# Performance work log

Hardware: AMD Instinct MI355X
Metric: run time of the kernel (lower is better)

## Reference

```python
import jax, jax.numpy as jnp
import numpy as np

N_BOX = 1000000


def box2corners(box):
    # box: (N,5) = x,y,w,h,alpha -> corners (N,4,2), order matches lilanxiao/Rotated_IoU
    x, y, w, h, a = (box[:, i] for i in range(5))
    dx = jnp.array([0.5, -0.5, -0.5, 0.5], box.dtype)
    dy = jnp.array([0.5, 0.5, -0.5, -0.5], box.dtype)
    cx = dx[None, :] * w[:, None]
    cy = dy[None, :] * h[:, None]
    c, s = jnp.cos(a)[:, None], jnp.sin(a)[:, None]
    rx = cx * c - cy * s + x[:, None]
    ry = cx * s + cy * c + y[:, None]
    return jnp.stack([rx, ry], axis=-1)


def edge_intersections(c1, c2):
    # all 4x4 edge-pair intersections; strict interior criterion (0<t<1, 0<u<1)
    p1, p2 = c1, jnp.roll(c1, -1, axis=1)
    p3, p4 = c2, jnp.roll(c2, -1, axis=1)
    x1, y1 = p1[:, :, None, 0], p1[:, :, None, 1]
    x2, y2 = p2[:, :, None, 0], p2[:, :, None, 1]
    x3, y3 = p3[:, None, :, 0], p3[:, None, :, 1]
    x4, y4 = p4[:, None, :, 0], p4[:, None, :, 1]
    num_t = (x2 - x1) * (y3 - y1) - (y2 - y1) * (x3 - x1)
    den_t = (x2 - x1) * (y3 - y4) - (y2 - y1) * (x3 - x4)
    t = jnp.where(den_t == 0., -1., num_t / jnp.where(den_t == 0., 1., den_t))
    mask_t = (t > 0.) & (t < 1.)
    num_u = (x4 - x3) * (y1 - y3) - (y4 - y3) * (x1 - x3)
    den_u = (x4 - x3) * (y1 - y2) - (y4 - y3) * (x1 - x2)
    u = jnp.where(den_u == 0., -1., num_u / jnp.where(den_u == 0., 1., den_u))
    mask = mask_t & (u > 0.) & (u < 1.)
    tx = x1 + t * (x2 - x1)
    ty = y1 + t * (y2 - y1)
    pts = jnp.stack([tx, ty], axis=-1) * mask[..., None]
    n = c1.shape[0]
    return pts.reshape(n, 16, 2), mask.reshape(n, 16)


def box_in_box(corners1, corners2):
    # projection test: is each corner of box1 inside rectangle box2
    a = corners2[:, 0:1, :]
    b = corners2[:, 1:2, :]
    d = corners2[:, 3:4, :]
    ab, ad, am = b - a, d - a, corners1 - a
    p_ab = (ab * am).sum(-1) / (ab * ab).sum(-1)
    p_ad = (ad * am).sum(-1) / (ad * ad).sum(-1)
    eps = 1e-6
    return (p_ab > -eps) & (p_ab < 1. + eps) & (p_ad > -eps) & (p_ad < 1. + eps)


def intersection_area(c1, c2):
    # convex intersection polygon: 24 candidate vertices, sort valid ones by angle, shoelace
    pts, m_int = edge_intersections(c1, c2)
    m1 = box_in_box(c1, c2)
    m2 = box_in_box(c2, c1)
    verts = jnp.concatenate([c1, c2, pts], axis=1)   # (N,24,2)
    mask = jnp.concatenate([m1, m2, m_int], axis=1)  # (N,24)
    k = mask.sum(axis=1)
    mean = (verts * mask[..., None]).sum(1, keepdims=True) / jnp.maximum(k, 1)[:, None, None]
    v = jnp.where(mask[..., None], verts - mean, 0.)
    ang = jnp.where(mask, jnp.arctan2(v[..., 1], v[..., 0]), 1e9)
    order = jnp.argsort(ang, axis=1)
    vs = jnp.take_along_axis(v, order[..., None], axis=1)
    pad = jnp.arange(24)[None, :, None] < k[:, None, None]
    vs = jnp.where(pad, vs, vs[:, 0:1, :])  # pad by repeating first valid vertex -> zero cross terms
    vn = jnp.roll(vs, -1, axis=1)
    cross = vs[..., 0] * vn[..., 1] - vs[..., 1] * vn[..., 0]
    return 0.5 * jnp.abs(cross.sum(axis=1))


def riou_loss(pred, target):
    # RIOUloss(reduction='none', loss_type='iou') -> cal_diou per-box loss, loss[0]
    rad_p = jnp.arctan2(pred[:, 4], pred[:, 5])
    rad_t = jnp.arctan2(target[:, 4], target[:, 5])
    b1 = jnp.concatenate([pred[:, :4], rad_p[:, None]], axis=1)
    b2 = jnp.concatenate([target[:, :4], rad_t[:, None]], axis=1)
    c1 = box2corners(b1)
    c2 = box2corners(b2)
    inter = intersection_area(c1, c2)
    area1 = b1[:, 2] * b1[:, 3]
    area2 = b2[:, 2] * b2[:, 3]
    union = area1 + area2 - inter
    iou = inter / union
    allc = jnp.concatenate([c1, c2], axis=1)  # (N,8,2) enclosing box (axis-aligned)
    wc = allc[..., 0].max(1) - allc[..., 0].min(1)
    hc = allc[..., 1].max(1) - allc[..., 1].min(1)
    c2diag = wc * wc + hc * hc
    d2 = (b1[:, 0] - b2[:, 0]) ** 2 + (b1[:, 1] - b2[:, 1]) ** 2
    return 1. - iou + d2 / c2diag


def setup_inputs() -> dict:
    key = jax.random.key(0)
    k1, k2, k3, k4 = jax.random.split(key, 4)
    n = N_BOX
    xy = jax.random.uniform(k1, (n, 2)) * 640.
    wh = jax.random.uniform(k2, (n, 2)) * 48. + 2.
    sc = jax.random.normal(k3, (n, 2)) + 0.1
    pred = jnp.concatenate([xy, wh, sc], axis=1)
    k5, k6, k7 = jax.random.split(k4, 3)
    t_xy = xy + jax.random.normal(k5, (n, 2)) * 8.
    t_wh = jnp.abs(wh * (1. + 0.2 * jax.random.normal(k6, (n, 2)))) + 1.
    t_sc = sc + 0.3 * jax.random.normal(k7, (n, 2))
    target = jnp.concatenate([t_xy, t_wh, t_sc], axis=1)
    return {"pred": pred, "target": target}


def reference(pred, target):
    return riou_loss(pred, target)
```

## Files before the change

### kernel.cpp

```cpp
#include <hip/hip_runtime.h>
#include <math.h>


#define FMUL __fmul_rn
#define FADD __fadd_rn
#define FSUB __fsub_rn
#define FDIV __fdiv_rn

__device__ __forceinline__ float rcpf_(float x) { return __builtin_amdgcn_rcpf(x); }

__global__
__attribute__((amdgpu_flat_work_group_size(256, 256), amdgpu_waves_per_eu(1)))
void riou_kernel(const float* __restrict__ pred,
                 const float* __restrict__ tgt,
                 float* __restrict__ out, int n)
{
    int i = blockIdx.x * blockDim.x + threadIdx.x;
    if (i >= n) return;

    const float2* p2 = (const float2*)(pred + 6 * (size_t)i);
    const float2* q2 = (const float2*)(tgt  + 6 * (size_t)i);
    float2 pa = p2[0], pb = p2[1], pc2 = p2[2];
    float2 qa = q2[0], qb = q2[1], qc2 = q2[2];
    const float px = pa.x, py = pa.y, pw = pb.x, ph = pb.y;
    const float qx = qa.x, qy = qa.y, qw = qb.x, qh = qb.y;

    float rad1 = atan2f(pc2.x, pc2.y);
    float cA = cosf(rad1), sA = sinf(rad1);
    float rad2 = atan2f(qc2.x, qc2.y);
    float cB = cosf(rad2), sB = sinf(rad2);

    const float ddx[4] = {0.5f, -0.5f, -0.5f, 0.5f};
    const float ddy[4] = {0.5f, 0.5f, -0.5f, -0.5f};
    float c1x[4], c1y[4], c2x[4], c2y[4];
#pragma unroll
    for (int j = 0; j < 4; j++) {
        float cx = FMUL(ddx[j], pw), cy = FMUL(ddy[j], ph);
        c1x[j] = FADD(FSUB(FMUL(cx, cA), FMUL(cy, sA)), px);
        c1y[j] = FADD(FADD(FMUL(cx, sA), FMUL(cy, cA)), py);
        float dx2 = FMUL(ddx[j], qw), dy2 = FMUL(ddy[j], qh);
        c2x[j] = FADD(FSUB(FMUL(dx2, cB), FMUL(dy2, sB)), qx);
        c2y[j] = FADD(FADD(FMUL(dx2, sB), FMUL(dy2, cB)), qy);
    }

    float minx = c1x[0], maxx = c1x[0], miny = c1y[0], maxy = c1y[0];
#pragma unroll
    for (int j = 1; j < 4; j++) {
        minx = fminf(minx, c1x[j]); maxx = fmaxf(maxx, c1x[j]);
        miny = fminf(miny, c1y[j]); maxy = fmaxf(maxy, c1y[j]);
    }
#pragma unroll
    for (int j = 0; j < 4; j++) {
        minx = fminf(minx, c2x[j]); maxx = fmaxf(maxx, c2x[j]);
        miny = fminf(miny, c2y[j]); maxy = fmaxf(maxy, c2y[j]);
    }
    float wcb = FSUB(maxx, minx), hcb = FSUB(maxy, miny);
    float c2d = FADD(FMUL(wcb, wcb), FMUL(hcb, hcb));
    float dxc = FSUB(px, qx), dyc = FSUB(py, qy);
    float d2 = FADD(FMUL(dxc, dxc), FMUL(dyc, dyc));

    float vx[24], vy[24];
    unsigned mbits = 0;
    float sx = 0.0f, sy = 0.0f;
    const float eps = 1e-6f;
    const float hieps = 1.0f + 1e-6f;

    {
        float ax = c2x[0], ay = c2y[0];
        float abx = FSUB(c2x[1], ax), aby = FSUB(c2y[1], ay);
        float adx = FSUB(c2x[3], ax), ady = FSUB(c2y[3], ay);
        float rab = rcpf_(FADD(FMUL(abx, abx), FMUL(aby, aby)));
        float rad = rcpf_(FADD(FMUL(adx, adx), FMUL(ady, ady)));
#pragma unroll
        for (int j = 0; j < 4; j++) {
            float amx = FSUB(c1x[j], ax), amy = FSUB(c1y[j], ay);
            float pab = FMUL(FADD(FMUL(abx, amx), FMUL(aby, amy)), rab);
            float pad = FMUL(FADD(FMUL(adx, amx), FMUL(ady, amy)), rad);
            int m = (pab > -eps) & (pab < hieps) & (pad > -eps) & (pad < hieps);
            vx[j] = c1x[j]; vy[j] = c1y[j];
            mbits |= (unsigned)m << j;
            sx = FADD(sx, m ? c1x[j] : 0.0f);
            sy = FADD(sy, m ? c1y[j] : 0.0f);
        }
    }
    {
        float ax = c1x[0], ay = c1y[0];
        float abx = FSUB(c1x[1], ax), aby = FSUB(c1y[1], ay);
        float adx = FSUB(c1x[3], ax), ady = FSUB(c1y[3], ay);
        float rab = rcpf_(FADD(FMUL(abx, abx), FMUL(aby, aby)));
        float rad = rcpf_(FADD(FMUL(adx, adx), FMUL(ady, ady)));
#pragma unroll
        for (int j = 0; j < 4; j++) {
            float amx = FSUB(c2x[j], ax), amy = FSUB(c2y[j], ay);
            float pab = FMUL(FADD(FMUL(abx, amx), FMUL(aby, amy)), rab);
            float pad = FMUL(FADD(FMUL(adx, amx), FMUL(ady, amy)), rad);
            int m = (pab > -eps) & (pab < hieps) & (pad > -eps) & (pad < hieps);
            vx[4 + j] = c2x[j]; vy[4 + j] = c2y[j];
            mbits |= (unsigned)m << (4 + j);
            sx = FADD(sx, m ? c2x[j] : 0.0f);
            sy = FADD(sy, m ? c2y[j] : 0.0f);
        }
    }
    float fex[4], fey[4];
#pragma unroll
    for (int e2 = 0; e2 < 4; e2++) {
        fex[e2] = FSUB(c2x[(e2 + 1) & 3], c2x[e2]);
        fey[e2] = FSUB(c2y[(e2 + 1) & 3], c2y[e2]);
    }
#pragma unroll
    for (int e1 = 0; e1 < 4; e1++) {
        float x1 = c1x[e1], y1 = c1y[e1];
        float ex = FSUB(c1x[(e1 + 1) & 3], x1), ey = FSUB(c1y[(e1 + 1) & 3], y1);
#pragma unroll
        for (int e2 = 0; e2 < 4; e2++) {
            float dx31 = FSUB(c2x[e2], x1), dy31 = FSUB(c2y[e2], y1);
            float num_t = FSUB(FMUL(ex, dy31), FMUL(ey, dx31));
            float den_t = FSUB(FMUL(ey, fex[e2]), FMUL(ex, fey[e2]));
            float rd = rcpf_(den_t);
            float tq = FMUL(num_t, rd);
            float num_u = FSUB(FMUL(fey[e2], dx31), FMUL(fex[e2], dy31));
            float uq = FMUL(num_u, rd);
            int m = (tq > 0.0f) & (tq < 1.0f) & (uq < 0.0f) & (uq > -1.0f);
            float ix = FADD(x1, FMUL(tq, ex));
            float iy = FADD(y1, FMUL(tq, ey));
            int s = 8 + 4 * e1 + e2;
            vx[s] = ix; vy[s] = iy;
            mbits |= (unsigned)m << s;
            sx = FADD(sx, m ? ix : 0.0f);
            sy = FADD(sy, m ? iy : 0.0f);
        }
    }

    int k = __popc(mbits);

    float kk = (float)(k > 0 ? k : 1);
    float mx = FDIV(sx, kk), my = FDIV(sy, kk);

    unsigned pk[24];
#pragma unroll
    for (int j = 0; j < 24; j++) {
        int m = (mbits >> j) & 1u;
        float wx2 = FSUB(vx[j], mx);
        float wy2 = FSUB(vy[j], my);
        vx[j] = wx2; vy[j] = wy2;
        float dsum = FADD(fabsf(wx2), fabsf(wy2));
        float rs = (dsum > 0.0f) ? FMUL(wx2, rcpf_(dsum)) : 1.0f;
        float keyf = copysignf(FSUB(1.0f, rs), wy2);
        unsigned sb = __float_as_uint(keyf);
        unsigned u = sb ^ (unsigned)(((int)sb >> 31) | (int)0x80000000);
        pk[j] = m ? ((u & 0xFFFFFFE0u) | (unsigned)j)
                  : (0xFFFFFFE0u | (unsigned)j);
    }

    unsigned prevkey = 0xFFFFFFFFu;
    float firstx = 0.0f, firsty = 0.0f, prevx = 0.0f, prevy = 0.0f;
    float crs = 0.0f;
#pragma unroll
    for (int s = 0; s < 8; s++) {
        unsigned poff = prevkey + 1u;
        unsigned cb0, cb1, cb2, cb3;
        float cxx0, cxx1, cxx2, cxx3, cyy0, cyy1, cyy2, cyy3;
#pragma unroll
        for (int c = 0; c < 4; c++) {
            unsigned b = pk[6 * c] - poff;
            float bx = vx[6 * c], by = vy[6 * c];
#pragma unroll
            for (int t = 1; t < 6; t++) {
                int j = 6 * c + t;
                unsigned wj = pk[j] - poff;
                bool lt = wj < b;
                b  = lt ? wj : b;
                bx = lt ? vx[j] : bx;
                by = lt ? vy[j] : by;
            }
            if (c == 0) { cb0 = b; cxx0 = bx; cyy0 = by; }
            else if (c == 1) { cb1 = b; cxx1 = bx; cyy1 = by; }
            else if (c == 2) { cb2 = b; cxx2 = bx; cyy2 = by; }
            else { cb3 = b; cxx3 = bx; cyy3 = by; }
        }
        bool l01 = cb1 < cb0;
        unsigned b01 = l01 ? cb1 : cb0;
        float x01 = l01 ? cxx1 : cxx0, y01 = l01 ? cyy1 : cyy0;
        bool l23 = cb3 < cb2;
        unsigned b23 = l23 ? cb3 : cb2;
        float x23 = l23 ? cxx3 : cxx2, y23 = l23 ? cyy3 : cyy2;
        bool lf = b23 < b01;
        unsigned bw = lf ? b23 : b01;
        float bx = lf ? x23 : x01, by = lf ? y23 : y01;
        unsigned bestkey = bw + poff;
        bool act = s < k;
        bx = act ? bx : prevx;
        by = act ? by : prevy;
        if (s == 0) { firstx = bx; firsty = by; }
        else {
            crs = FADD(crs, FSUB(FMUL(prevx, by), FMUL(prevy, bx)));
        }
        prevx = bx; prevy = by; prevkey = bestkey;
    }
    for (int s = 8; s < k; s++) {
        unsigned poff = prevkey + 1u;
        unsigned best = pk[0] - poff;
        float bx = vx[0], by = vy[0];
#pragma unroll
        for (int j = 1; j < 24; j++) {
            unsigned wj = pk[j] - poff;
            bool lt = wj < best;
            best = lt ? wj : best;
            bx = lt ? vx[j] : bx;
            by = lt ? vy[j] : by;
        }
        crs = FADD(crs, FSUB(FMUL(prevx, by), FMUL(prevy, bx)));
        prevx = bx; prevy = by; prevkey = best + poff;
    }
    crs = FADD(crs, FSUB(FMUL(prevx, firsty), FMUL(prevy, firstx)));
    float inter = FMUL(0.5f, fabsf(crs));

    float area1 = FMUL(pw, ph), area2 = FMUL(qw, qh);
    float uni = FSUB(FADD(area1, area2), inter);
    float iou = FMUL(inter, rcpf_(uni));

    out[i] = FADD(FSUB(1.0f, iou), FMUL(d2, rcpf_(c2d)));
}

extern "C" void kernel_launch(void* const* d_in, const int* in_sizes, int n_in,
                              void* d_out, int out_size, void* d_ws, size_t ws_size,
                              hipStream_t stream) {
    const float* pred = (const float*)d_in[0];
    const float* tgt  = (const float*)d_in[1];
    float* out = (float*)d_out;
    int n = in_sizes[0] / 6;
    int block = 256;
    int grid = (n + block - 1) / block;
    riou_kernel<<<grid, block, 0, stream>>>(pred, tgt, out, n);
}
```

Before: 127.9 us.

## Replace repeated selection with sorting network and stage vertices in LDS

Replaces the 8-round full min-selection over 24 packed angle keys with a sorting network: three sorted groups of 8, merged to keep the lowest 8, then vertices are gathered by index. Vertex coordinates move from register arrays into a per-thread shared-memory array so they can be fetched by the sorted index without carrying x/y through every compare. The goal is fewer compare-select instructions and less register pressure. The cost is extra LDS stores and loads. The rare case of more than 8 vertices falls back to a min-search over the remaining keys, which removes each chosen key after use.

```diff
diff --git a/kernel.cpp b/kernel.cpp
--- a/kernel.cpp
+++ b/kernel.cpp
@@ -8,6 +8,23 @@
 #define FDIV __fdiv_rn
 
 __device__ __forceinline__ float rcpf_(float x) { return __builtin_amdgcn_rcpf(x); }
+
+#define CE(A,B) do { unsigned _x = pk[A], _y = pk[B]; \
+                     pk[A] = _x < _y ? _x : _y; pk[B] = _x < _y ? _y : _x; } while (0)
+
+#define SORT8(o) do { \
+    CE(o+0,o+1); CE(o+2,o+3); CE(o+0,o+2); CE(o+1,o+3); CE(o+1,o+2); \
+    CE(o+4,o+5); CE(o+6,o+7); CE(o+4,o+6); CE(o+5,o+7); CE(o+5,o+6); \
+    CE(o+0,o+4); CE(o+1,o+5); CE(o+2,o+6); CE(o+3,o+7); \
+    CE(o+2,o+4); CE(o+3,o+5); \
+    CE(o+1,o+2); CE(o+3,o+4); CE(o+5,o+6); } while (0)
+
+#define MERGE_LOW8(o) do { \
+    CE(0,o+7); CE(1,o+6); CE(2,o+5); CE(3,o+4); \
+    CE(4,o+3); CE(5,o+2); CE(6,o+1); CE(7,o+0); \
+    CE(0,4); CE(1,5); CE(2,6); CE(3,7); \
+    CE(0,2); CE(1,3); CE(4,6); CE(5,7); \
+    CE(0,1); CE(2,3); CE(4,5); CE(6,7); } while (0)
 
 __global__
 __attribute__((amdgpu_flat_work_group_size(256, 256), amdgpu_waves_per_eu(1)))
@@ -15,7 +32,9 @@
                  const float* __restrict__ tgt,
                  float* __restrict__ out, int n)
 {
-    int i = blockIdx.x * blockDim.x + threadIdx.x;
+    __shared__ float2 vlds[24][256];
+    const int tid = threadIdx.x;
+    int i = blockIdx.x * blockDim.x + tid;
     if (i >= n) return;
 
     const float2* p2 = (const float2*)(pred + 6 * (size_t)i);
@@ -59,7 +78,6 @@
     float dxc = FSUB(px, qx), dyc = FSUB(py, qy);
     float d2 = FADD(FMUL(dxc, dxc), FMUL(dyc, dyc));
 
-    float vx[24], vy[24];
     unsigned mbits = 0;
     float sx = 0.0f, sy = 0.0f;
     const float eps = 1e-6f;
@@ -77,7 +95,6 @@
             float pab = FMUL(FADD(FMUL(abx, amx), FMUL(aby, amy)), rab);
             float pad = FMUL(FADD(FMUL(adx, amx), FMUL(ady, amy)), rad);
             int m = (pab > -eps) & (pab < hieps) & (pad > -eps) & (pad < hieps);
-            vx[j] = c1x[j]; vy[j] = c1y[j];
             mbits |= (unsigned)m << j;
             sx = FADD(sx, m ? c1x[j] : 0.0f);
             sy = FADD(sy, m ? c1y[j] : 0.0f);
@@ -95,7 +112,6 @@
             float pab = FMUL(FADD(FMUL(abx, amx), FMUL(aby, amy)), rab);
             float pad = FMUL(FADD(FMUL(adx, amx), FMUL(ady, amy)), rad);
             int m = (pab > -eps) & (pab < hieps) & (pad > -eps) & (pad < hieps);
-            vx[4 + j] = c2x[j]; vy[4 + j] = c2y[j];
             mbits |= (unsigned)m << (4 + j);
             sx = FADD(sx, m ? c2x[j] : 0.0f);
             sy = FADD(sy, m ? c2y[j] : 0.0f);
@@ -124,7 +140,7 @@
             float ix = FADD(x1, FMUL(tq, ex));
             float iy = FADD(y1, FMUL(tq, ey));
             int s = 8 + 4 * e1 + e2;
-            vx[s] = ix; vy[s] = iy;
+            vlds[s][tid] = make_float2(ix, iy);
             mbits |= (unsigned)m << s;
             sx = FADD(sx, m ? ix : 0.0f);
             sy = FADD(sy, m ? iy : 0.0f);
@@ -140,9 +156,13 @@
 #pragma unroll
     for (int j = 0; j < 24; j++) {
         int m = (mbits >> j) & 1u;
-        float wx2 = FSUB(vx[j], mx);
-        float wy2 = FSUB(vy[j], my);
-        vx[j] = wx2; vy[j] = wy2;
+        float rx, ry;
+        if (j < 4)      { rx = c1x[j];     ry = c1y[j];     }
+        else if (j < 8) { rx = c2x[j - 4]; ry = c2y[j - 4]; }
+        else            { float2 v = vlds[j][tid]; rx = v.x; ry = v.y; }
+        float wx2 = FSUB(rx, mx);
+        float wy2 = FSUB(ry, my);
+        vlds[j][tid] = make_float2(wx2, wy2);
         float dsum = FADD(fabsf(wx2), fabsf(wy2));
         float rs = (dsum > 0.0f) ? FMUL(wx2, rcpf_(dsum)) : 1.0f;
         float keyf = copysignf(FSUB(1.0f, rs), wy2);
@@ -152,65 +172,43 @@
                   : (0xFFFFFFE0u | (unsigned)j);
     }
 
-    unsigned prevkey = 0xFFFFFFFFu;
+    SORT8(0);
+    SORT8(8);
+    SORT8(16);
+    MERGE_LOW8(8);
+    MERGE_LOW8(16);
+
+    float gxv[8], gyv[8];
+#pragma unroll
+    for (int s = 0; s < 8; s++) {
+        float2 v = vlds[pk[s] & 31u][tid];
+        gxv[s] = v.x; gyv[s] = v.y;
+    }
+
     float firstx = 0.0f, firsty = 0.0f, prevx = 0.0f, prevy = 0.0f;
     float crs = 0.0f;
 #pragma unroll
     for (int s = 0; s < 8; s++) {
-        unsigned poff = prevkey + 1u;
-        unsigned cb0, cb1, cb2, cb3;
-        float cxx0, cxx1, cxx2, cxx3, cyy0, cyy1, cyy2, cyy3;
-#pragma unroll
-        for (int c = 0; c < 4; c++) {
-            unsigned b = pk[6 * c] - poff;
-            float bx = vx[6 * c], by = vy[6 * c];
-#pragma unroll
-            for (int t = 1; t < 6; t++) {
-                int j = 6 * c + t;
-                unsigned wj = pk[j] - poff;
-                bool lt = wj < b;
-                b  = lt ? wj : b;
-                bx = lt ? vx[j] : bx;
-                by = lt ? vy[j] : by;
-            }
-            if (c == 0) { cb0 = b; cxx0 = bx; cyy0 = by; }
-            else if (c == 1) { cb1 = b; cxx1 = bx; cyy1 = by; }
-            else if (c == 2) { cb2 = b; cxx2 = bx; cyy2 = by; }
-            else { cb3 = b; cxx3 = bx; cyy3 = by; }
-        }
-        bool l01 = cb1 < cb0;
-        unsigned b01 = l01 ? cb1 : cb0;
-        float x01 = l01 ? cxx1 : cxx0, y01 = l01 ? cyy1 : cyy0;
-        bool l23 = cb3 < cb2;
-        unsigned b23 = l23 ? cb3 : cb2;
-        float x23 = l23 ? cxx3 : cxx2, y23 = l23 ? cyy3 : cyy2;
-        bool lf = b23 < b01;
-        unsigned bw = lf ? b23 : b01;
-        float bx = lf ? x23 : x01, by = lf ? y23 : y01;
-        unsigned bestkey = bw + poff;
         bool act = s < k;
-        bx = act ? bx : prevx;
-        by = act ? by : prevy;
+        float bx = act ? gxv[s] : prevx;
+        float by = act ? gyv[s] : prevy;
         if (s == 0) { firstx = bx; firsty = by; }
         else {
             crs = FADD(crs, FSUB(FMUL(prevx, by), FMUL(prevy, bx)));
         }
-        prevx = bx; prevy = by; prevkey = bestkey;
-    }
-    for (int s = 8; s < k; s++) {
-        unsigned poff = prevkey + 1u;
-        unsigned best = pk[0] - poff;
-        float bx = vx[0], by = vy[0];
-#pragma unroll
-        for (int j = 1; j < 24; j++) {
-            unsigned wj = pk[j] - poff;
-            bool lt = wj < best;
-            best = lt ? wj : best;
-            bx = lt ? vx[j] : bx;
-            by = lt ? vy[j] : by;
-        }
-        crs = FADD(crs, FSUB(FMUL(prevx, by), FMUL(prevy, bx)));
-        prevx = bx; prevy = by; prevkey = best + poff;
+        prevx = bx; prevy = by;
+    }
+    if (k > 8) {
+        for (int s = 8; s < k; s++) {
+            unsigned mn = pk[8];
+#pragma unroll
+            for (int j = 9; j < 24; j++) mn = (pk[j] < mn) ? pk[j] : mn;
+            float2 v = vlds[mn & 31u][tid];
+            crs = FADD(crs, FSUB(FMUL(prevx, v.y), FMUL(prevy, v.x)));
+            prevx = v.x; prevy = v.y;
+#pragma unroll
+            for (int j = 8; j < 24; j++) if (pk[j] == mn) pk[j] = 0xFFFFFFFFu;
+        }
     }
     crs = FADD(crs, FSUB(FMUL(prevx, firsty), FMUL(prevy, firstx)));
     float inter = FMUL(0.5f, fabsf(crs));
```

Measured after the change: 113.0 us. -11.7%, faster.
